# Kernel optimization log

Hardware: AMD Instinct MI355X
Metric: run time of the kernel (lower is better)

The kernel has to match this reference:

```python
import jax, jax.numpy as jnp
import numpy as np

DIM = 512
WIN = 7
HEADS = 16
N = WIN * WIN            # 49 tokens per window
NW = 64                  # windows per image (56/7)^2
BATCH = 32               # images
B_ = BATCH * NW          # 2048 window-batches
TABLE = (2 * WIN - 1) ** 2  # 169


def _relative_position_index(win):
    # Faithful to the TF construction in __init__.
    coords = np.stack(np.meshgrid(np.arange(win), np.arange(win), indexing='ij'))
    coords = coords.reshape(2, -1).T                      # [N, 2]
    rel = coords[:, None, :] - coords[None, :, :]          # [N, N, 2]
    rel = rel + (win - 1)
    idx = rel[..., 0] * (2 * win - 1) + rel[..., 1]        # [N, N]
    return jnp.asarray(idx, dtype=jnp.int32)


def setup_inputs() -> dict:
    key = jax.random.key(0)
    ks = jax.random.split(key, 7)
    x = jax.random.normal(ks[0], (B_, N, DIM), dtype=jnp.float32)
    # shifted-window additive mask: 0 where allowed, -100 where blocked
    mask = jnp.where(jax.random.uniform(ks[1], (NW, N, N)) < 0.8, 0.0, -100.0).astype(jnp.float32)
    qkv_w = jax.random.normal(ks[2], (DIM, 3 * DIM), dtype=jnp.float32) * 0.02
    qkv_b = jax.random.normal(ks[3], (3 * DIM,), dtype=jnp.float32) * 0.02
    proj_w = jax.random.normal(ks[4], (DIM, DIM), dtype=jnp.float32) * 0.02
    proj_b = jax.random.normal(ks[5], (DIM,), dtype=jnp.float32) * 0.02
    rel_table = jax.random.normal(ks[6], (TABLE, HEADS), dtype=jnp.float32) * 0.02
    rel_index = _relative_position_index(WIN)
    return {"x": x, "mask": mask, "qkv_w": qkv_w, "qkv_b": qkv_b,
            "proj_w": proj_w, "proj_b": proj_b,
            "rel_table": rel_table, "rel_index": rel_index}


def reference(x, mask, qkv_w, qkv_b, proj_w, proj_b, rel_table, rel_index):
    B, n, C = x.shape
    hd = C // HEADS
    scale = hd ** (-0.5)
    # qkv projection -> [3, B, H, N, hd]
    qkv = (x @ qkv_w + qkv_b).reshape(B, n, 3, HEADS, hd).transpose(2, 0, 3, 1, 4)
    q, k, v = qkv[0] * scale, qkv[1], qkv[2]
    attn = jnp.einsum('bhnd,bhmd->bhnm', q, k)             # [B, H, N, N]
    # relative position bias gather: [N*N] -> [N, N, H] -> [H, N, N]
    bias = rel_table[rel_index.reshape(-1)].reshape(n, n, HEADS).transpose(2, 0, 1)
    attn = attn + bias[None]
    nW = mask.shape[0]
    attn = attn.reshape(B // nW, nW, HEADS, n, n) + mask[None, :, None]
    attn = attn.reshape(-1, HEADS, n, n)
    attn = jax.nn.softmax(attn, axis=-1)
    out = jnp.einsum('bhnm,bhmd->bhnd', attn, v)           # [B, H, N, hd]
    out = out.transpose(0, 2, 1, 3).reshape(B, n, C)
    return out @ proj_w + proj_b
```

## Files before the change

### kernel.cpp

```cpp
#include <hip/hip_runtime.h>

typedef unsigned short ushort_t;
typedef short short8 __attribute__((ext_vector_type(8)));
typedef float f32x4 __attribute__((ext_vector_type(4)));
typedef unsigned short ushort4v __attribute__((ext_vector_type(4)));

__device__ __forceinline__ ushort_t f2bf(float f) {
    unsigned int u = __float_as_uint(f);
    u = (u + 0x7fffu + ((u >> 16) & 1u)) >> 16;
    return (ushort_t)u;
}

__device__ __forceinline__ void async16(void* lds, const void* g) {
    __builtin_amdgcn_global_load_lds(
        (const __attribute__((address_space(1))) unsigned int*)g,
        (__attribute__((address_space(3))) unsigned int*)lds, 16, 0, 0);
}

__global__ void conv_x_kernel(const float* __restrict__ in, ushort_t* __restrict__ out) {
    int i = blockIdx.x * 256 + threadIdx.x;
    float4 v = ((const float4*)in)[i];
    ushort4v o;
    o.x = f2bf(v.x); o.y = f2bf(v.y); o.z = f2bf(v.z); o.w = f2bf(v.w);
    ((ushort4v*)out)[i] = o;
}

__global__ void prep_weights(const float* __restrict__ qkv_w, const float* __restrict__ proj_w,
                             ushort_t* __restrict__ wtq, ushort_t* __restrict__ wtp) {
    int o = blockIdx.x * 256 + threadIdx.x;
    if (o < 1536 * 512) {
        int n = o >> 9, k = o & 511;
        wtq[o] = f2bf(qkv_w[k * 1536 + n]);
    }
    if (o < 512 * 512) {
        int n = o >> 9, k = o & 511;
        wtp[o] = f2bf(proj_w[k * 512 + n]);
    }
}

__global__ void build_cm(const float* __restrict__ mask, const float* __restrict__ rel_table,
                         const int* __restrict__ rel_index, float* __restrict__ cm) {
    int o = blockIdx.x * 256 + threadIdx.x;
    int c = o & 63, r = (o >> 6) & 63, h = (o >> 12) & 15, w = o >> 16;
    float v = -30000.0f;
    if (r < 49 && c < 49)
        v = rel_table[rel_index[r * 49 + c] * 16 + h] + mask[w * 2401 + r * 49 + c];
    cm[o] = v;
}

template<int NSTR, bool QKV>
__global__ __launch_bounds__(256, 2)
void gemm_bt(const ushort_t* __restrict__ A, const ushort_t* __restrict__ Bt,
             const float* __restrict__ bias, void* __restrict__ out,
             int M, int K)
{
    __shared__ alignas(16) ushort_t As[128 * 32];
    __shared__ alignas(16) ushort_t Bs[128 * 32];
    const int tid = threadIdx.x;
    const int wid = tid >> 6;
    const int lane = tid & 63;
    const int lr = lane & 15;
    const int lk = lane >> 4;
    const int n0 = blockIdx.x << 7;
    const int m0 = blockIdx.y << 7;
    const int wr = (wid >> 1) << 6;
    const int wc = (wid & 1) << 6;

    f32x4 acc[4][4];
#pragma unroll
    for (int i = 0; i < 4; ++i)
#pragma unroll
        for (int j = 0; j < 4; ++j)
#pragma unroll
            for (int r = 0; r < 4; ++r) acc[i][j][r] = 0.f;

    const int KT = K >> 5;
    for (int kt = 0; kt < KT; ++kt) {
        const int kb = kt << 5;
#pragma unroll
        for (int t = 0; t < 2; ++t) {
            const int cb = t * 256 + wid * 64;
            const int c = cb + lane;
            const int row = c >> 2;
            const int kc = (c & 3) ^ ((row >> 1) & 3);
            async16((char*)As + cb * 16, A + (size_t)(m0 + row) * K + kb + kc * 8);
            async16((char*)Bs + cb * 16, Bt + (size_t)(n0 + row) * K + kb + kc * 8);
        }
        __syncthreads();
        const int swz = ((lr >> 1) & 3) << 3;
        short8 af[4], bf[4];
#pragma unroll
        for (int i = 0; i < 4; ++i) af[i] = *(const short8*)&As[(wr + i * 16 + lr) * 32 + ((lk * 8) ^ swz)];
#pragma unroll
        for (int j = 0; j < 4; ++j) bf[j] = *(const short8*)&Bs[(wc + j * 16 + lr) * 32 + ((lk * 8) ^ swz)];
#pragma unroll
        for (int i = 0; i < 4; ++i)
#pragma unroll
            for (int j = 0; j < 4; ++j)
                acc[i][j] = __builtin_amdgcn_mfma_f32_16x16x32_bf16(bf[j], af[i], acc[i][j], 0, 0, 0);
        __syncthreads();
    }

#pragma unroll
    for (int i = 0; i < 4; ++i) {
        const int row = m0 + wr + i * 16 + lr;
#pragma unroll
        for (int j = 0; j < 4; ++j) {
            const int col = n0 + wc + j * 16 + lk * 4;
            const float4 bv = *(const float4*)&bias[col];
            float v0 = acc[i][j][0] + bv.x;
            float v1 = acc[i][j][1] + bv.y;
            float v2 = acc[i][j][2] + bv.z;
            float v3 = acc[i][j][3] + bv.w;
            if (QKV) {
                if (col < 512) {
                    v0 *= 0.17677669529663689f; v1 *= 0.17677669529663689f;
                    v2 *= 0.17677669529663689f; v3 *= 0.17677669529663689f;
                }
                ushort4v o;
                o.x = f2bf(v0); o.y = f2bf(v1); o.z = f2bf(v2); o.w = f2bf(v3);
                *(ushort4v*)&((ushort_t*)out)[(size_t)row * NSTR + col] = o;
            } else {
                float4 o; o.x = v0; o.y = v1; o.z = v2; o.w = v3;
                *(float4*)&((float*)out)[(size_t)row * NSTR + col] = o;
            }
        }
    }
}

#define PL_STRIDE 80
#define VT_STRIDE 88
__global__ __launch_bounds__(256, 2)
void attn_kernel(const ushort_t* __restrict__ qkv, const float* __restrict__ cm,
                 ushort_t* __restrict__ out)
{
    __shared__ alignas(16) char smem[4 * 64 * PL_STRIDE * 2 + 4 * 32 * VT_STRIDE * 2];
    float* cmf = (float*)smem;
    ushort_t* Pl = (ushort_t*)smem;
    ushort_t* vT = (ushort_t*)(smem + 4 * 64 * PL_STRIDE * 2);

    const int ig = blockIdx.x, w = blockIdx.y, h = blockIdx.z;
    const int tid = threadIdx.x;
    const int wid = tid >> 6, lane = tid & 63;
    const int lr = lane & 15, lk = lane >> 4;
    const int b = (ig * 4 + wid) * 64 + w;

    const float* cmsrc = cm + ((size_t)(w * 16 + h) << 12);
    for (int t = tid; t < 4096; t += 256)
        cmf[(t >> 6) * 65 + (t & 63)] = cmsrc[t];
    __syncthreads();

    const size_t base = (size_t)b * 49 * 1536 + h * 32;

    short8 aq[4], bk[4];
#pragma unroll
    for (int i = 0; i < 4; ++i) {
        int n = i * 16 + lr; n = n > 48 ? 48 : n;
        aq[i] = *(const short8*)&qkv[base + (size_t)n * 1536 + lk * 8];
    }
#pragma unroll
    for (int j = 0; j < 4; ++j) {
        int m = j * 16 + lr; m = m > 48 ? 48 : m;
        bk[j] = *(const short8*)&qkv[base + 512 + (size_t)m * 1536 + lk * 8];
    }

    f32x4 s[4][4];
#pragma unroll
    for (int i = 0; i < 4; ++i)
#pragma unroll
        for (int j = 0; j < 4; ++j)
#pragma unroll
            for (int r = 0; r < 4; ++r) s[i][j][r] = 0.f;
#pragma unroll
    for (int i = 0; i < 4; ++i)
#pragma unroll
        for (int j = 0; j < 4; ++j)
            s[i][j] = __builtin_amdgcn_mfma_f32_16x16x32_bf16(aq[i], bk[j], s[i][j], 0, 0, 0);

    short8 vv[4];
#pragma unroll
    for (int t = 0; t < 4; ++t)
#pragma unroll
        for (int e = 0; e < 8; ++e) vv[t][e] = 0;
    if (lane < 49) {
        const ushort_t* vp = &qkv[base + 1024 + (size_t)lane * 1536];
#pragma unroll
        for (int t = 0; t < 4; ++t) vv[t] = *(const short8*)(vp + t * 8);
    }
    ushort_t* vTw = vT + wid * 32 * VT_STRIDE;
#pragma unroll
    for (int t = 0; t < 4; ++t)
#pragma unroll
        for (int e = 0; e < 8; ++e)
            vTw[(t * 8 + e) * VT_STRIDE + lane] = (ushort_t)vv[t][e];

#pragma unroll
    for (int i = 0; i < 4; ++i) {
#pragma unroll
        for (int r = 0; r < 4; ++r) {
            const int row = i * 16 + lk * 4 + r;
            float v0 = s[i][0][r] + cmf[row * 65 + lr];
            float v1 = s[i][1][r] + cmf[row * 65 + 16 + lr];
            float v2 = s[i][2][r] + cmf[row * 65 + 32 + lr];
            float v3 = s[i][3][r] + cmf[row * 65 + 48 + lr];
            float mx = fmaxf(fmaxf(v0, v1), fmaxf(v2, v3));
#pragma unroll
            for (int t = 1; t < 16; t <<= 1) mx = fmaxf(mx, __shfl_xor(mx, t, 64));
            v0 = __expf(v0 - mx); v1 = __expf(v1 - mx);
            v2 = __expf(v2 - mx); v3 = __expf(v3 - mx);
            float sm = v0 + v1 + v2 + v3;
#pragma unroll
            for (int t = 1; t < 16; t <<= 1) sm += __shfl_xor(sm, t, 64);
            const float inv = 1.0f / sm;
            s[i][0][r] = v0 * inv; s[i][1][r] = v1 * inv;
            s[i][2][r] = v2 * inv; s[i][3][r] = v3 * inv;
        }
    }
    __syncthreads();

    ushort_t* Pw = Pl + wid * 64 * PL_STRIDE;
#pragma unroll
    for (int i = 0; i < 4; ++i)
#pragma unroll
        for (int j = 0; j < 4; ++j)
#pragma unroll
            for (int r = 0; r < 4; ++r)
                Pw[(i * 16 + lk * 4 + r) * PL_STRIDE + j * 16 + lr] = f2bf(s[i][j][r]);

    f32x4 o[4][2];
#pragma unroll
    for (int i = 0; i < 4; ++i)
#pragma unroll
        for (int jb = 0; jb < 2; ++jb)
#pragma unroll
            for (int r = 0; r < 4; ++r) o[i][jb][r] = 0.f;
#pragma unroll
    for (int ks = 0; ks < 2; ++ks) {
        short8 pa[4], vb[2];
#pragma unroll
        for (int i = 0; i < 4; ++i)
            pa[i] = *(const short8*)&Pw[(i * 16 + lr) * PL_STRIDE + ks * 32 + lk * 8];
#pragma unroll
        for (int jb = 0; jb < 2; ++jb)
            vb[jb] = *(const short8*)&vTw[(jb * 16 + lr) * VT_STRIDE + ks * 32 + lk * 8];
#pragma unroll
        for (int i = 0; i < 4; ++i)
#pragma unroll
            for (int jb = 0; jb < 2; ++jb)
                o[i][jb] = __builtin_amdgcn_mfma_f32_16x16x32_bf16(vb[jb], pa[i], o[i][jb], 0, 0, 0);
    }

    const size_t obase = (size_t)b * 49 * 512 + h * 32;
#pragma unroll
    for (int i = 0; i < 4; ++i) {
        const int n = i * 16 + lr;
        if (n < 49) {
#pragma unroll
            for (int jb = 0; jb < 2; ++jb) {
                ushort4v ov;
                ov.x = f2bf(o[i][jb][0]); ov.y = f2bf(o[i][jb][1]);
                ov.z = f2bf(o[i][jb][2]); ov.w = f2bf(o[i][jb][3]);
                *(ushort4v*)&out[obase + (size_t)n * 512 + jb * 16 + lk * 4] = ov;
            }
        }
    }
}

extern "C" void kernel_launch(void* const* d_in, const int* in_sizes, int n_in,
                              void* d_out, int out_size, void* d_ws, size_t ws_size,
                              hipStream_t stream)
{
    const float* x         = (const float*)d_in[0];
    const float* mask      = (const float*)d_in[1];
    const float* qkv_w     = (const float*)d_in[2];
    const float* qkv_b     = (const float*)d_in[3];
    const float* proj_w    = (const float*)d_in[4];
    const float* proj_b    = (const float*)d_in[5];
    const float* rel_table = (const float*)d_in[6];
    const int*   rel_index = (const int*)d_in[7];

    char* ws = (char*)d_ws;
    ushort_t* xb  = (ushort_t*)ws;
    ushort_t* qkv = (ushort_t*)(ws + 102760448);
    ushort_t* wtq = (ushort_t*)(ws + 411041792);
    ushort_t* wtp = (ushort_t*)(ws + 412614656);
    float*    cm  = (float*)  (ws + 413138944);

    conv_x_kernel<<<50176, 256, 0, stream>>>(x, xb);
    prep_weights<<<3072, 256, 0, stream>>>(qkv_w, proj_w, wtq, wtp);
    build_cm<<<16384, 256, 0, stream>>>(mask, rel_table, rel_index, cm);

    gemm_bt<1536, true><<<dim3(12, 784), 256, 0, stream>>>(xb, wtq, qkv_b, qkv, 100352, 512);

    attn_kernel<<<dim3(8, 64, 16), 256, 0, stream>>>(qkv, cm, xb);

    gemm_bt<512, false><<<dim3(4, 784), 256, 0, stream>>>(xb, wtp, proj_b, d_out, 100352, 512);
}
```

Before: 671.9 us.

## Replace 128x128 GEMM with double-buffered 256x256 tile, 8-wave pipelined kernel

Swaps the simple single-buffered 128x128 GEMM for a 512-thread kernel that computes 256x256 tiles with K-chunks of 64. LDS is double-buffered, and async global-to-LDS loads for the next chunk are interleaved with MFMA phases that use barriers and s_setprio. Blocks are remapped across XCD-sized chunks, and the attention grid order is permuted so windows vary fastest. The goal is more reuse per loaded byte and overlap of loads with math, at the cost of higher register and LDS pressure (128 KB LDS per block).

```diff
diff --git a/kernel.cpp b/kernel.cpp
--- a/kernel.cpp
+++ b/kernel.cpp
@@ -48,70 +48,123 @@
     cm[o] = v;
 }
 
-template<int NSTR, bool QKV>
-__global__ __launch_bounds__(256, 2)
-void gemm_bt(const ushort_t* __restrict__ A, const ushort_t* __restrict__ Bt,
-             const float* __restrict__ bias, void* __restrict__ out,
-             int M, int K)
+
+#define STAGE(ldsbase, gbase) do {                                              \
+    _Pragma("unroll")                                                           \
+    for (int j_ = 0; j_ < 2; ++j_) {                                            \
+        const int idx_ = j_ * 512 + tid;                                        \
+        const int row_ = idx_ >> 3;                                             \
+        const int c0_  = (idx_ & 7) << 3;                                       \
+        const int sc_  = c0_ ^ (((row_ >> 1) & 3) << 3);                        \
+        async16((char*)(ldsbase) + idx_ * 16, (gbase) + (size_t)row_ * K + sc_);\
+    }                                                                           \
+} while (0)
+
+#define VMNOP ((void)0)
+#define VM0 asm volatile("s_waitcnt vmcnt(0)" ::: "memory")
+#define NOSTAGE ((void)0)
+
+#define PHASE(buf, mh, nh, WAITST, ...) do {                                    \
+    short8 af_[4][2], bf_[2][2];                                                \
+    _Pragma("unroll")                                                           \
+    for (int f_ = 0; f_ < 4; ++f_) {                                            \
+        const int ar_ = wr + ((mh) * 4 + f_) * 16 + lr;                         \
+        _Pragma("unroll")                                                       \
+        for (int ks_ = 0; ks_ < 2; ++ks_)                                       \
+            af_[f_][ks_] = *(const short8*)&As[buf][ar_ * 64 + ((ks_ * 32 + lk * 8) ^ swz)]; \
+    }                                                                           \
+    _Pragma("unroll")                                                           \
+    for (int g_ = 0; g_ < 2; ++g_) {                                            \
+        const int br_ = wc + ((nh) * 2 + g_) * 16 + lr;                         \
+        _Pragma("unroll")                                                       \
+        for (int ks_ = 0; ks_ < 2; ++ks_)                                       \
+            bf_[g_][ks_] = *(const short8*)&Bs[buf][br_ * 64 + ((ks_ * 32 + lk * 8) ^ swz)]; \
+    }                                                                           \
+    __VA_ARGS__;                                                                \
+    __builtin_amdgcn_s_barrier();                                               \
+    asm volatile("s_waitcnt lgkmcnt(0)" ::: "memory");                          \
+    __builtin_amdgcn_sched_barrier(0);                                          \
+    __builtin_amdgcn_s_setprio(1);                                              \
+    _Pragma("unroll")                                                           \
+    for (int f_ = 0; f_ < 4; ++f_)                                              \
+        _Pragma("unroll")                                                       \
+        for (int g_ = 0; g_ < 2; ++g_)                                          \
+            _Pragma("unroll")                                                   \
+            for (int ks_ = 0; ks_ < 2; ++ks_)                                   \
+                acc[(mh) * 4 + f_][(nh) * 2 + g_] = __builtin_amdgcn_mfma_f32_16x16x32_bf16( \
+                    bf_[g_][ks_], af_[f_][ks_], acc[(mh) * 4 + f_][(nh) * 2 + g_], 0, 0, 0); \
+    __builtin_amdgcn_s_setprio(0);                                              \
+    WAITST;                                                                     \
+    __builtin_amdgcn_s_barrier();                                               \
+} while (0)
+
+template<int NB_N, int NSTR, bool QKV, int K>
+__global__ __launch_bounds__(512, 2)
+void gemm8(const ushort_t* __restrict__ A, const ushort_t* __restrict__ Bt,
+           const float* __restrict__ bias, void* __restrict__ out)
 {
-    __shared__ alignas(16) ushort_t As[128 * 32];
-    __shared__ alignas(16) ushort_t Bs[128 * 32];
+    __shared__ alignas(16) ushort_t As[2][256 * 64];
+    __shared__ alignas(16) ushort_t Bs[2][256 * 64];
+
     const int tid = threadIdx.x;
-    const int wid = tid >> 6;
-    const int lane = tid & 63;
-    const int lr = lane & 15;
-    const int lk = lane >> 4;
-    const int n0 = blockIdx.x << 7;
-    const int m0 = blockIdx.y << 7;
-    const int wr = (wid >> 1) << 6;
-    const int wc = (wid & 1) << 6;
-
-    f32x4 acc[4][4];
-#pragma unroll
-    for (int i = 0; i < 4; ++i)
-#pragma unroll
-        for (int j = 0; j < 4; ++j)
-#pragma unroll
-            for (int r = 0; r < 4; ++r) acc[i][j][r] = 0.f;
-
-    const int KT = K >> 5;
-    for (int kt = 0; kt < KT; ++kt) {
-        const int kb = kt << 5;
-#pragma unroll
-        for (int t = 0; t < 2; ++t) {
-            const int cb = t * 256 + wid * 64;
-            const int c = cb + lane;
-            const int row = c >> 2;
-            const int kc = (c & 3) ^ ((row >> 1) & 3);
-            async16((char*)As + cb * 16, A + (size_t)(m0 + row) * K + kb + kc * 8);
-            async16((char*)Bs + cb * 16, Bt + (size_t)(n0 + row) * K + kb + kc * 8);
-        }
-        __syncthreads();
-        const int swz = ((lr >> 1) & 3) << 3;
-        short8 af[4], bf[4];
-#pragma unroll
-        for (int i = 0; i < 4; ++i) af[i] = *(const short8*)&As[(wr + i * 16 + lr) * 32 + ((lk * 8) ^ swz)];
-#pragma unroll
-        for (int j = 0; j < 4; ++j) bf[j] = *(const short8*)&Bs[(wc + j * 16 + lr) * 32 + ((lk * 8) ^ swz)];
-#pragma unroll
-        for (int i = 0; i < 4; ++i)
-#pragma unroll
-            for (int j = 0; j < 4; ++j)
-                acc[i][j] = __builtin_amdgcn_mfma_f32_16x16x32_bf16(bf[j], af[i], acc[i][j], 0, 0, 0);
-        __syncthreads();
-    }
-
-#pragma unroll
-    for (int i = 0; i < 4; ++i) {
-        const int row = m0 + wr + i * 16 + lr;
-#pragma unroll
-        for (int j = 0; j < 4; ++j) {
-            const int col = n0 + wc + j * 16 + lk * 4;
+    const int wid = tid >> 6, lane = tid & 63;
+    const int lr = lane & 15, lk = lane >> 4;
+    const int wr = (wid >> 2) * 128;
+    const int wc = (wid & 3) * 64;
+    const int swz = ((lr >> 1) & 3) << 3;
+
+    const int chunk = gridDim.x >> 3;
+    const int wg = ((int)blockIdx.x & 7) * chunk + ((int)blockIdx.x >> 3);
+    const int nb = wg % NB_N;
+    const int mb = wg / NB_N;
+    const int m0 = mb << 8, n0 = nb << 8;
+
+    const size_t a0 = (size_t)m0 * K;
+    const size_t a1 = (size_t)(m0 + 128) * K;
+    const size_t b0 = (size_t)n0 * K;
+    const size_t b1 = (size_t)(n0 + 128) * K;
+
+    f32x4 acc[8][4];
+#pragma unroll
+    for (int f = 0; f < 8; ++f)
+#pragma unroll
+        for (int g = 0; g < 4; ++g)
+#pragma unroll
+            for (int r = 0; r < 4; ++r) acc[f][g][r] = 0.f;
+
+    STAGE(&As[0][0],    A  + a0);
+    STAGE(&As[0][8192], A  + a1);
+    STAGE(&Bs[0][0],    Bt + b0);
+    STAGE(&Bs[0][8192], Bt + b1);
+    VM0;
+    __builtin_amdgcn_s_barrier();
+
+    const int NI = K >> 7;
+    for (int i = 0; i < NI; ++i) {
+        const int ck = (2 * i + 1) << 6;
+        const int cn = (2 * i + 2) << 6;
+        const bool more = (i < NI - 1);
+        PHASE(0, 0, 0, VMNOP, { STAGE(&As[1][0], A + a0 + ck); STAGE(&As[1][8192], A + a1 + ck); });
+        PHASE(0, 0, 1, VMNOP, { STAGE(&Bs[1][0], Bt + b0 + ck); STAGE(&Bs[1][8192], Bt + b1 + ck); });
+        PHASE(0, 1, 0, VMNOP, NOSTAGE);
+        PHASE(0, 1, 1, VM0,   NOSTAGE);
+        PHASE(1, 0, 0, VMNOP, { if (more) { STAGE(&As[0][0], A + a0 + cn); STAGE(&As[0][8192], A + a1 + cn); } });
+        PHASE(1, 0, 1, VMNOP, { if (more) { STAGE(&Bs[0][0], Bt + b0 + cn); STAGE(&Bs[0][8192], Bt + b1 + cn); } });
+        PHASE(1, 1, 0, VMNOP, NOSTAGE);
+        PHASE(1, 1, 1, VM0,   NOSTAGE);
+    }
+
+#pragma unroll
+    for (int f = 0; f < 8; ++f) {
+        const int row = m0 + wr + f * 16 + lr;
+#pragma unroll
+        for (int g = 0; g < 4; ++g) {
+            const int col = n0 + wc + g * 16 + lk * 4;
             const float4 bv = *(const float4*)&bias[col];
-            float v0 = acc[i][j][0] + bv.x;
-            float v1 = acc[i][j][1] + bv.y;
-            float v2 = acc[i][j][2] + bv.z;
-            float v3 = acc[i][j][3] + bv.w;
+            float v0 = acc[f][g][0] + bv.x;
+            float v1 = acc[f][g][1] + bv.y;
+            float v2 = acc[f][g][2] + bv.z;
+            float v3 = acc[f][g][3] + bv.w;
             if (QKV) {
                 if (col < 512) {
                     v0 *= 0.17677669529663689f; v1 *= 0.17677669529663689f;
@@ -139,7 +192,7 @@
     ushort_t* Pl = (ushort_t*)smem;
     ushort_t* vT = (ushort_t*)(smem + 4 * 64 * PL_STRIDE * 2);
 
-    const int ig = blockIdx.x, w = blockIdx.y, h = blockIdx.z;
+    const int w = blockIdx.x, h = blockIdx.y, ig = blockIdx.z;
     const int tid = threadIdx.x;
     const int wid = tid >> 6, lane = tid & 63;
     const int lr = lane & 15, lk = lane >> 4;
@@ -290,9 +343,9 @@
     prep_weights<<<3072, 256, 0, stream>>>(qkv_w, proj_w, wtq, wtp);
     build_cm<<<16384, 256, 0, stream>>>(mask, rel_table, rel_index, cm);
 
-    gemm_bt<1536, true><<<dim3(12, 784), 256, 0, stream>>>(xb, wtq, qkv_b, qkv, 100352, 512);
-
-    attn_kernel<<<dim3(8, 64, 16), 256, 0, stream>>>(qkv, cm, xb);
-
-    gemm_bt<512, false><<<dim3(4, 784), 256, 0, stream>>>(xb, wtp, proj_b, d_out, 100352, 512);
-}
+    gemm8<6, 1536, true, 512><<<2352, 512, 0, stream>>>(xb, wtq, qkv_b, qkv);
+
+    attn_kernel<<<dim3(64, 16, 8), 256, 0, stream>>>(qkv, cm, xb);
+
+    gemm8<2, 512, false, 512><<<784, 512, 0, stream>>>(xb, wtp, proj_b, d_out);
+}
```

Result: slower. 700.0 us (+4.2%).

## Replace LDS-staged GEMM with register double-buffered direct-load GEMM

Applied to the files above, without the earlier changes.

Replaces the LDS-staged GEMM with one where each wave loads its A (128 rows) and B (64 cols) fragments straight from global memory into registers. The kernel double-buffers over K in steps of 32 and drops all barriers, using a 128x256 block tile. This removes the LDS round-trip and the per-step __syncthreads stalls. The cost is that A fragments are no longer shared across waves: each wave reloads the full A tile, so global and L2 traffic rises and register pressure climbs (acc 8x4 plus two fragment buffers), which may spill under launch_bounds(256,2). Separately, the attention grid is reordered so window and head vary fastest, which changes cache locality for the mask/bias and qkv reads.

```diff
diff --git a/kernel.cpp b/kernel.cpp
--- a/kernel.cpp
+++ b/kernel.cpp
@@ -9,12 +9,6 @@
     unsigned int u = __float_as_uint(f);
     u = (u + 0x7fffu + ((u >> 16) & 1u)) >> 16;
     return (ushort_t)u;
-}
-
-__device__ __forceinline__ void async16(void* lds, const void* g) {
-    __builtin_amdgcn_global_load_lds(
-        (const __attribute__((address_space(1))) unsigned int*)g,
-        (__attribute__((address_space(3))) unsigned int*)lds, 16, 0, 0);
 }
 
 __global__ void conv_x_kernel(const float* __restrict__ in, ushort_t* __restrict__ out) {
@@ -48,70 +42,72 @@
     cm[o] = v;
 }
 
-template<int NSTR, bool QKV>
+
+#define LOADG(af, bf, kb) do {                                                  \
+    _Pragma("unroll")                                                           \
+    for (int f_ = 0; f_ < 8; ++f_)                                              \
+        af[f_] = *(const short8*)(Ap + (size_t)f_ * 16 * K + (kb));             \
+    _Pragma("unroll")                                                           \
+    for (int g_ = 0; g_ < 4; ++g_)                                              \
+        bf[g_] = *(const short8*)(Bp + (size_t)g_ * 16 * K + (kb));             \
+} while (0)
+
+#define MFMAT(af, bf) do {                                                      \
+    _Pragma("unroll")                                                           \
+    for (int f_ = 0; f_ < 8; ++f_)                                              \
+        _Pragma("unroll")                                                       \
+        for (int g_ = 0; g_ < 4; ++g_)                                          \
+            acc[f_][g_] = __builtin_amdgcn_mfma_f32_16x16x32_bf16(              \
+                bf[g_], af[f_], acc[f_][g_], 0, 0, 0);                          \
+} while (0)
+
+template<int NSTR, bool QKV, int K>
 __global__ __launch_bounds__(256, 2)
-void gemm_bt(const ushort_t* __restrict__ A, const ushort_t* __restrict__ Bt,
-             const float* __restrict__ bias, void* __restrict__ out,
-             int M, int K)
+void gemm_reg(const ushort_t* __restrict__ A, const ushort_t* __restrict__ Bt,
+              const float* __restrict__ bias, void* __restrict__ out)
 {
-    __shared__ alignas(16) ushort_t As[128 * 32];
-    __shared__ alignas(16) ushort_t Bs[128 * 32];
     const int tid = threadIdx.x;
-    const int wid = tid >> 6;
-    const int lane = tid & 63;
-    const int lr = lane & 15;
-    const int lk = lane >> 4;
-    const int n0 = blockIdx.x << 7;
-    const int m0 = blockIdx.y << 7;
-    const int wr = (wid >> 1) << 6;
-    const int wc = (wid & 1) << 6;
-
-    f32x4 acc[4][4];
-#pragma unroll
-    for (int i = 0; i < 4; ++i)
-#pragma unroll
-        for (int j = 0; j < 4; ++j)
-#pragma unroll
-            for (int r = 0; r < 4; ++r) acc[i][j][r] = 0.f;
-
-    const int KT = K >> 5;
-    for (int kt = 0; kt < KT; ++kt) {
-        const int kb = kt << 5;
-#pragma unroll
-        for (int t = 0; t < 2; ++t) {
-            const int cb = t * 256 + wid * 64;
-            const int c = cb + lane;
-            const int row = c >> 2;
-            const int kc = (c & 3) ^ ((row >> 1) & 3);
-            async16((char*)As + cb * 16, A + (size_t)(m0 + row) * K + kb + kc * 8);
-            async16((char*)Bs + cb * 16, Bt + (size_t)(n0 + row) * K + kb + kc * 8);
-        }
-        __syncthreads();
-        const int swz = ((lr >> 1) & 3) << 3;
-        short8 af[4], bf[4];
-#pragma unroll
-        for (int i = 0; i < 4; ++i) af[i] = *(const short8*)&As[(wr + i * 16 + lr) * 32 + ((lk * 8) ^ swz)];
-#pragma unroll
-        for (int j = 0; j < 4; ++j) bf[j] = *(const short8*)&Bs[(wc + j * 16 + lr) * 32 + ((lk * 8) ^ swz)];
-#pragma unroll
-        for (int i = 0; i < 4; ++i)
-#pragma unroll
-            for (int j = 0; j < 4; ++j)
-                acc[i][j] = __builtin_amdgcn_mfma_f32_16x16x32_bf16(bf[j], af[i], acc[i][j], 0, 0, 0);
-        __syncthreads();
-    }
-
-#pragma unroll
-    for (int i = 0; i < 4; ++i) {
-        const int row = m0 + wr + i * 16 + lr;
-#pragma unroll
-        for (int j = 0; j < 4; ++j) {
-            const int col = n0 + wc + j * 16 + lk * 4;
+    const int wid = tid >> 6, lane = tid & 63;
+    const int lr = lane & 15, lk = lane >> 4;
+    const int m0 = (int)blockIdx.y << 7;
+    const int n0 = ((int)blockIdx.x << 8) + (wid << 6);
+
+    const ushort_t* Ap = A  + (size_t)(m0 + lr) * K + lk * 8;
+    const ushort_t* Bp = Bt + (size_t)(n0 + lr) * K + lk * 8;
+
+    f32x4 acc[8][4];
+#pragma unroll
+    for (int f = 0; f < 8; ++f)
+#pragma unroll
+        for (int g = 0; g < 4; ++g)
+#pragma unroll
+            for (int r = 0; r < 4; ++r) acc[f][g][r] = 0.f;
+
+    short8 af0[8], bf0[4], af1[8], bf1[4];
+    LOADG(af0, bf0, 0);
+    LOADG(af1, bf1, 32);
+
+#pragma unroll 1
+    for (int kb = 0; kb + 96 < K; kb += 64) {
+        MFMAT(af0, bf0);
+        LOADG(af0, bf0, kb + 64);
+        MFMAT(af1, bf1);
+        LOADG(af1, bf1, kb + 96);
+    }
+    MFMAT(af0, bf0);
+    MFMAT(af1, bf1);
+
+#pragma unroll
+    for (int f = 0; f < 8; ++f) {
+        const int row = m0 + f * 16 + lr;
+#pragma unroll
+        for (int g = 0; g < 4; ++g) {
+            const int col = n0 + g * 16 + lk * 4;
             const float4 bv = *(const float4*)&bias[col];
-            float v0 = acc[i][j][0] + bv.x;
-            float v1 = acc[i][j][1] + bv.y;
-            float v2 = acc[i][j][2] + bv.z;
-            float v3 = acc[i][j][3] + bv.w;
+            float v0 = acc[f][g][0] + bv.x;
+            float v1 = acc[f][g][1] + bv.y;
+            float v2 = acc[f][g][2] + bv.z;
+            float v3 = acc[f][g][3] + bv.w;
             if (QKV) {
                 if (col < 512) {
                     v0 *= 0.17677669529663689f; v1 *= 0.17677669529663689f;
@@ -139,7 +135,7 @@
     ushort_t* Pl = (ushort_t*)smem;
     ushort_t* vT = (ushort_t*)(smem + 4 * 64 * PL_STRIDE * 2);
 
-    const int ig = blockIdx.x, w = blockIdx.y, h = blockIdx.z;
+    const int w = blockIdx.x, h = blockIdx.y, ig = blockIdx.z;
     const int tid = threadIdx.x;
     const int wid = tid >> 6, lane = tid & 63;
     const int lr = lane & 15, lk = lane >> 4;
@@ -290,9 +286,9 @@
     prep_weights<<<3072, 256, 0, stream>>>(qkv_w, proj_w, wtq, wtp);
     build_cm<<<16384, 256, 0, stream>>>(mask, rel_table, rel_index, cm);
 
-    gemm_bt<1536, true><<<dim3(12, 784), 256, 0, stream>>>(xb, wtq, qkv_b, qkv, 100352, 512);
-
-    attn_kernel<<<dim3(8, 64, 16), 256, 0, stream>>>(qkv, cm, xb);
-
-    gemm_bt<512, false><<<dim3(4, 784), 256, 0, stream>>>(xb, wtp, proj_b, d_out, 100352, 512);
-}
+    gemm_reg<1536, true, 512><<<dim3(6, 784), 256, 0, stream>>>(xb, wtq, qkv_b, qkv);
+
+    attn_kernel<<<dim3(64, 16, 8), 256, 0, stream>>>(qkv, cm, xb);
+
+    gemm_reg<512, false, 512><<<dim3(2, 784), 256, 0, stream>>>(xb, wtp, proj_b, d_out);
+}
```

Measured after the change: 939.4 us. +39.8%, slower.
